# Optimization experiments

Hardware: AMD Instinct MI355X
Metric: run time of the kernel (lower is better)

The kernel has to match this reference:

```python
import jax, jax.numpy as jnp
import numpy as np

V, E, H = 32000, 64, 256
B, T = 8, 512


def _lstm_dir(xs, Wi, Wh, b, reverse):
    """xs: [T, B, D] time-major. Returns hs: [T, B, H].
    Gate layout (custom cell): [f, i, g, o] along the 4H axis."""
    hsz = Wh.shape[0]
    x_proj = jnp.einsum('tbd,dg->tbg', xs, Wi) + b  # precompute input GEMM

    def step(carry, xp_t):
        h, c = carry
        gates = xp_t + h @ Wh
        f = jax.nn.sigmoid(gates[:, :hsz])
        i = jax.nn.sigmoid(gates[:, hsz:2 * hsz])
        g = jnp.tanh(gates[:, 2 * hsz:3 * hsz])
        o = jax.nn.sigmoid(gates[:, 3 * hsz:])
        c = f * c + i * g
        h = o * jnp.tanh(c)
        return (h, c), h

    bsz = xs.shape[1]
    init = (jnp.zeros((bsz, hsz), xs.dtype), jnp.zeros((bsz, hsz), xs.dtype))
    _, hs = jax.lax.scan(step, init, x_proj, reverse=reverse)
    return hs


def setup_inputs() -> dict:
    key = jax.random.key(0)
    ks = jax.random.split(key, 8)
    x = jax.random.randint(ks[0], (B, T), 0, V, dtype=jnp.int32)
    emb = jax.random.normal(ks[1], (V, E), jnp.float32)
    Wi_f = jax.random.normal(ks[2], (E, 4 * H), jnp.float32) / np.sqrt(E)
    Wh_f = jax.random.normal(ks[3], (H, 4 * H), jnp.float32) / np.sqrt(H)
    b_f = jnp.zeros((4 * H,), jnp.float32).at[H:2 * H].set(1.0)
    Wi_b = jax.random.normal(ks[4], (E, 4 * H), jnp.float32) / np.sqrt(E)
    Wh_b = jax.random.normal(ks[5], (H, 4 * H), jnp.float32) / np.sqrt(H)
    b_b = jnp.zeros((4 * H,), jnp.float32).at[H:2 * H].set(1.0)
    W_out = jax.random.normal(ks[6], (2 * H, V), jnp.float32) / np.sqrt(2 * H)
    b_out = jnp.zeros((V,), jnp.float32)
    return {"x": x, "emb": emb, "Wi_f": Wi_f, "Wh_f": Wh_f, "b_f": b_f,
            "Wi_b": Wi_b, "Wh_b": Wh_b, "b_b": b_b,
            "W_out": W_out, "b_out": b_out}


def reference(x, emb, Wi_f, Wh_f, b_f, Wi_b, Wh_b, b_b, W_out, b_out):
    embeds = emb[x]                      # [B, T, E]
    xs = jnp.swapaxes(embeds, 0, 1)      # [T, B, E] time-major for scan
    h_fwd = _lstm_dir(xs, Wi_f, Wh_f, b_f, reverse=False)  # [T, B, H]
    h_bwd = _lstm_dir(xs, Wi_b, Wh_b, b_b, reverse=True)   # [T, B, H]
    h2 = jnp.concatenate([h_fwd, h_bwd], axis=-1)           # [T, B, 2H]
    h2 = jnp.swapaxes(h2, 0, 1)                             # [B, T, 2H]
    logits = jnp.einsum('btd,dv->btv', h2, W_out) + b_out   # [B, T, V]
    return logits
```

## Files before the change

kernel.cpp:

```cpp
#include <hip/hip_runtime.h>
#include <hip/hip_bf16.h>

#define T_LEN 512
#define BATCH 8
#define HID   256
#define G4    1024
#define EMBD  64
#define VOC   32000
#define KDIM  512

typedef __attribute__((ext_vector_type(8))) short bh8;
typedef __attribute__((ext_vector_type(4))) short s4v;
typedef __attribute__((ext_vector_type(4))) float fx4;

__device__ inline unsigned short f2b(float f) {
    unsigned u = __builtin_bit_cast(unsigned, f);
    unsigned r = (u + 0x7fffu + ((u >> 16) & 1u)) >> 16;
    return (unsigned short)r;
}

__device__ inline float sigm(float x) { return 1.f / (1.f + __expf(-x)); }
__device__ inline float tanh_f(float x) {
    float e = __expf(-2.f * fabsf(x));
    float r = (1.f - e) / (1.f + e);
    return copysignf(r, x);
}

__device__ inline void gload_lds16(const void* g, void* l) {
    __builtin_amdgcn_global_load_lds(
        (const __attribute__((address_space(1))) void*)g,
        (__attribute__((address_space(3))) void*)l, 16, 0, 0);
}

__global__ __launch_bounds__(256, 2) void prep_kernel(
    const int* __restrict__ x, const float* __restrict__ emb,
    const float* __restrict__ Wi_f, const float* __restrict__ Wh_f, const float* __restrict__ b_f,
    const float* __restrict__ Wi_b, const float* __restrict__ Wh_b, const float* __restrict__ b_b,
    const float* __restrict__ W_out,
    float* __restrict__ xp_f, float* __restrict__ xp_b,
    unsigned short* __restrict__ WhT_f, unsigned short* __restrict__ WhT_b,
    unsigned short* __restrict__ Wt)
{
    __shared__ float lds[128 * 65];
    __shared__ int xidx[16];
    const int bid = blockIdx.x, tid = threadIdx.x;

    if (bid < 256) {
        const int dir = bid >> 7, b2 = bid & 127;
        const float* Wh = dir ? Wh_b : Wh_f;
        unsigned short* WhT = dir ? WhT_b : WhT_f;
        const int k0 = (b2 >> 4) * 32, n0 = (b2 & 15) * 64;
        for (int it = 0; it < 8; ++it) {
            int idx = it * 256 + tid, kk = idx >> 6, nn = idx & 63;
            lds[kk * 65 + nn] = Wh[(k0 + kk) * G4 + n0 + nn];
        }
        __syncthreads();
        int nn = tid >> 2, kq = (tid & 3) * 8;
        bh8 v;
        #pragma unroll
        for (int j = 0; j < 8; ++j) v[j] = (short)f2b(lds[(kq + j) * 65 + nn]);
        *(bh8*)&WhT[(size_t)(n0 + nn) * HID + k0 + kq] = v;
    } else if (bid < 2256) {
        const int b2 = bid - 256;
        const int k0 = (b2 / 500) * 128, n0 = (b2 % 500) * 64;
        for (int it = 0; it < 32; ++it) {
            int idx = it * 256 + tid, kk = idx >> 6, nn = idx & 63;
            lds[kk * 65 + nn] = W_out[(size_t)(k0 + kk) * VOC + n0 + nn];
        }
        __syncthreads();
        const int kq = (tid & 15) * 8;
        #pragma unroll
        for (int g = 0; g < 4; ++g) {
            int nn = (tid >> 4) + g * 16;
            bh8 v;
            #pragma unroll
            for (int j = 0; j < 8; ++j) v[j] = (short)f2b(lds[(kq + j) * 65 + nn]);
            *(bh8*)&Wt[(size_t)(n0 + nn) * KDIM + k0 + kq] = v;
        }
    } else {
        const int b2 = bid - 2256;
        const int dir = b2 >> 8, rb = b2 & 255;
        const float* Wi = dir ? Wi_b : Wi_f;
        const float* bias = dir ? b_b : b_f;
        float* xp = dir ? xp_b : xp_f;
        const int f0 = rb * 16;
        if (tid < 16) {
            int f = f0 + tid, t = f >> 3, b = f & 7;
            xidx[tid] = x[b * T_LEN + t];
        }
        __syncthreads();
        {
            int rr = tid >> 4, e4 = (tid & 15) * 4;
            const float* er = emb + (size_t)xidx[rr] * EMBD + e4;
            lds[rr * 64 + e4 + 0] = er[0];
            lds[rr * 64 + e4 + 1] = er[1];
            lds[rr * 64 + e4 + 2] = er[2];
            lds[rr * 64 + e4 + 3] = er[3];
        }
        __syncthreads();
        const int g0 = tid * 4;
        float acc[16][4];
        float b0 = bias[g0], b1 = bias[g0 + 1], b2b = bias[g0 + 2], b3 = bias[g0 + 3];
        #pragma unroll
        for (int rr = 0; rr < 16; ++rr) {
            acc[rr][0] = b0; acc[rr][1] = b1; acc[rr][2] = b2b; acc[rr][3] = b3;
        }
        for (int e = 0; e < 64; ++e) {
            const float* wp = Wi + e * G4 + g0;
            float w0 = wp[0], w1 = wp[1], w2 = wp[2], w3 = wp[3];
            #pragma unroll
            for (int rr = 0; rr < 16; ++rr) {
                float xv = lds[rr * 64 + e];
                acc[rr][0] += xv * w0; acc[rr][1] += xv * w1;
                acc[rr][2] += xv * w2; acc[rr][3] += xv * w3;
            }
        }
        #pragma unroll
        for (int rr = 0; rr < 16; ++rr) {
            float* dst = xp + (size_t)(f0 + rr) * G4 + g0;
            dst[0] = acc[rr][0]; dst[1] = acc[rr][1];
            dst[2] = acc[rr][2]; dst[3] = acc[rr][3];
        }
    }
}

__global__ __launch_bounds__(1024, 4) void lstm_kernel(
    const float* __restrict__ xp_f, const float* __restrict__ xp_b,
    const unsigned short* __restrict__ WhT_f, const unsigned short* __restrict__ WhT_b,
    unsigned short* __restrict__ h2)
{
    const int dir = blockIdx.x;
    const float* xp = dir ? xp_b : xp_f;
    const unsigned short* WhT = dir ? WhT_b : WhT_f;
    const int tid = threadIdx.x;
    const int w = tid >> 6, lane = tid & 63, quad = lane >> 4, l15 = lane & 15;
    const int colBase = w * 64;

    __shared__ unsigned short hlds[16 * 264];
    __shared__ float gbuf[4 * 8 * 256];

    for (int i = tid; i < 16 * 264; i += 1024) hlds[i] = 0;

    bh8 bfr[4][8];
    #pragma unroll
    for (int nt = 0; nt < 4; ++nt)
        #pragma unroll
        for (int kt = 0; kt < 8; ++kt)
            bfr[nt][kt] = *(const bh8*)&WhT[(size_t)(colBase + nt * 16 + l15) * HID + kt * 32 + quad * 8];

    fx4 c = (fx4){0.f, 0.f, 0.f, 0.f};
    __syncthreads();

    for (int s = 0; s < T_LEN; ++s) {
        const int t = dir ? (T_LEN - 1 - s) : s;

        fx4 acc[4];
        #pragma unroll
        for (int nt = 0; nt < 4; ++nt) {
            if (quad < 2) {
                const float* p = xp + ((size_t)t * BATCH + quad * 4) * G4 + colBase + nt * 16 + l15;
                acc[nt][0] = p[0]; acc[nt][1] = p[G4]; acc[nt][2] = p[2 * G4]; acc[nt][3] = p[3 * G4];
            } else {
                acc[nt] = (fx4){0.f, 0.f, 0.f, 0.f};
            }
        }
        bh8 af[8];
        #pragma unroll
        for (int kt = 0; kt < 8; ++kt)
            af[kt] = *(const bh8*)&hlds[l15 * 264 + kt * 32 + quad * 8];
        #pragma unroll
        for (int nt = 0; nt < 4; ++nt)
            #pragma unroll
            for (int kt = 0; kt < 8; ++kt)
                acc[nt] = __builtin_amdgcn_mfma_f32_16x16x32_bf16(af[kt], bfr[nt][kt], acc[nt], 0, 0, 0);

        #pragma unroll
        for (int nt = 0; nt < 4; ++nt) {
            const int col = colBase + nt * 16 + l15;
            const int gt = col >> 8, hc = col & 255;
            if (quad < 2) {
                #pragma unroll
                for (int v = 0; v < 4; ++v) {
                    float xv = acc[nt][v];
                    float a = (gt == 2) ? tanh_f(xv) : sigm(xv);
                    gbuf[gt * 2048 + (quad * 4 + v) * 256 + hc] = a;
                }
            }
        }
        __syncthreads();

        if (tid < 512) {
            const int b = tid >> 6, hc0 = (tid & 63) * 4;
            const fx4 fv = *(const fx4*)&gbuf[0 * 2048 + b * 256 + hc0];
            const fx4 iv = *(const fx4*)&gbuf[1 * 2048 + b * 256 + hc0];
            const fx4 gv = *(const fx4*)&gbuf[2 * 2048 + b * 256 + hc0];
            const fx4 ov = *(const fx4*)&gbuf[3 * 2048 + b * 256 + hc0];
            s4v hv;
            #pragma unroll
            for (int j = 0; j < 4; ++j) {
                c[j] = fv[j] * c[j] + iv[j] * gv[j];
                float h = ov[j] * tanh_f(c[j]);
                hv[j] = (short)f2b(h);
            }
            *(s4v*)&hlds[b * 264 + hc0] = hv;
            *(s4v*)&h2[((size_t)b * T_LEN + t) * KDIM + dir * HID + hc0] = hv;
        }
        __syncthreads();
    }
}

__global__ __launch_bounds__(256, 2) void gemm_kernel(
    const unsigned short* __restrict__ A,
    const unsigned short* __restrict__ Bt,
    const float* __restrict__ b_out,
    float* __restrict__ out)
{
    const int bid = blockIdx.x;
    const int nb = bid % 250, mb = bid / 250;
    const int tid = threadIdx.x;
    const int wv = tid >> 6, lane = tid & 63, quad = lane >> 4, l15 = lane & 15;
    const int mrow0 = (wv >> 1) * 64, ncol0 = (wv & 1) * 64;

    __shared__ unsigned short smA[128 * 32];
    __shared__ unsigned short smB[128 * 32];

    fx4 acc[4][4];
    #pragma unroll
    for (int i = 0; i < 4; ++i)
        #pragma unroll
        for (int j = 0; j < 4; ++j) acc[i][j] = (fx4){0.f, 0.f, 0.f, 0.f};

    for (int kb = 0; kb < 16; ++kb) {
        __syncthreads();
        #pragma unroll
        for (int i = 0; i < 2; ++i) {
            const int f = ((i * 4 + wv) * 64 + lane) * 16;
            const int r = f >> 6, cb = f & 63;
            const char* ga = (const char*)A + ((size_t)(mb * 128 + r) * KDIM + kb * 32) * 2 + cb;
            gload_lds16(ga, (char*)smA + (i * 4 + wv) * 1024);
            const char* gb = (const char*)Bt + ((size_t)(nb * 128 + r) * KDIM + kb * 32) * 2 + cb;
            gload_lds16(gb, (char*)smB + (i * 4 + wv) * 1024);
        }
        __syncthreads();
        bh8 a[4], b[4];
        #pragma unroll
        for (int mt = 0; mt < 4; ++mt)
            a[mt] = *(const bh8*)&smA[(mrow0 + mt * 16 + l15) * 32 + quad * 8];
        #pragma unroll
        for (int nt = 0; nt < 4; ++nt)
            b[nt] = *(const bh8*)&smB[(ncol0 + nt * 16 + l15) * 32 + quad * 8];
        #pragma unroll
        for (int mt = 0; mt < 4; ++mt)
            #pragma unroll
            for (int nt = 0; nt < 4; ++nt)
                acc[mt][nt] = __builtin_amdgcn_mfma_f32_16x16x32_bf16(a[mt], b[nt], acc[mt][nt], 0, 0, 0);
    }

    float bia[4];
    #pragma unroll
    for (int nt = 0; nt < 4; ++nt)
        bia[nt] = b_out[nb * 128 + ncol0 + nt * 16 + l15];
    #pragma unroll
    for (int mt = 0; mt < 4; ++mt) {
        const int grow0 = mb * 128 + mrow0 + mt * 16 + quad * 4;
        #pragma unroll
        for (int nt = 0; nt < 4; ++nt) {
            const int gcol = nb * 128 + ncol0 + nt * 16 + l15;
            #pragma unroll
            for (int v = 0; v < 4; ++v)
                out[(size_t)(grow0 + v) * VOC + gcol] = acc[mt][nt][v] + bia[nt];
        }
    }
}

extern "C" void kernel_launch(void* const* d_in, const int* in_sizes, int n_in,
                              void* d_out, int out_size, void* d_ws, size_t ws_size,
                              hipStream_t stream) {
    const int*   x     = (const int*)d_in[0];
    const float* emb   = (const float*)d_in[1];
    const float* Wi_f  = (const float*)d_in[2];
    const float* Wh_f  = (const float*)d_in[3];
    const float* b_f   = (const float*)d_in[4];
    const float* Wi_b  = (const float*)d_in[5];
    const float* Wh_b  = (const float*)d_in[6];
    const float* b_b   = (const float*)d_in[7];
    const float* W_out = (const float*)d_in[8];
    const float* b_out = (const float*)d_in[9];
    float* out = (float*)d_out;

    char* ws = (char*)d_ws;
    float* xp_f          = (float*)(ws);
    float* xp_b          = (float*)(ws + 16777216);
    unsigned short* WhT_f = (unsigned short*)(ws + 33554432);
    unsigned short* WhT_b = (unsigned short*)(ws + 34078720);
    unsigned short* Wt    = (unsigned short*)(ws + 34603008);
    unsigned short* h2    = (unsigned short*)(ws + 67371008);

    prep_kernel<<<2768, 256, 0, stream>>>(x, emb, Wi_f, Wh_f, b_f, Wi_b, Wh_b, b_b,
                                          W_out, xp_f, xp_b, WhT_f, WhT_b, Wt);
    lstm_kernel<<<2, 1024, 0, stream>>>(xp_f, xp_b, WhT_f, WhT_b, h2);
    gemm_kernel<<<8000, 256, 0, stream>>>(h2, Wt, b_out, out);
}
```

Before: 4.764 ms.

## Split each LSTM direction across two workgroups with global h exchange

Each LSTM direction now runs on two 512-thread workgroups, each owning half of the hidden units. All four gates for a hidden unit are kept in one lane so the cell update happens in registers, which removes the gbuf LDS round trip and one barrier per step. The half-h vectors are exchanged every step through global memory, using per-step atomic flags that the workgroups spin on. The xp layout is changed to batch-innermost so the next step's input projection can be prefetched as fx4 loads. The risk is the cross-CU handshake latency on every step, and the spin loop gives up after a fixed iteration count instead of failing.

```diff
diff --git a/kernel.cpp b/kernel.cpp
--- a/kernel.cpp
+++ b/kernel.cpp
@@ -39,13 +39,17 @@
     const float* __restrict__ W_out,
     float* __restrict__ xp_f, float* __restrict__ xp_b,
     unsigned short* __restrict__ WhT_f, unsigned short* __restrict__ WhT_b,
-    unsigned short* __restrict__ Wt)
+    unsigned short* __restrict__ Wt,
+    unsigned int* __restrict__ flags)
 {
     __shared__ float lds[128 * 65];
     __shared__ int xidx[16];
     const int bid = blockIdx.x, tid = threadIdx.x;
 
     if (bid < 256) {
+        if (bid == 0) {
+            for (int i = tid; i < 2 * T_LEN; i += 256) flags[i] = 0;
+        }
         const int dir = bid >> 7, b2 = bid & 127;
         const float* Wh = dir ? Wh_b : Wh_f;
         unsigned short* WhT = dir ? WhT_b : WhT_f;
@@ -117,95 +121,140 @@
         }
         #pragma unroll
         for (int rr = 0; rr < 16; ++rr) {
-            float* dst = xp + (size_t)(f0 + rr) * G4 + g0;
-            dst[0] = acc[rr][0]; dst[1] = acc[rr][1];
-            dst[2] = acc[rr][2]; dst[3] = acc[rr][3];
+            const int f = f0 + rr, tt = f >> 3, bb = f & 7;
+            float* dst = xp + ((size_t)tt * G4 + g0) * 8 + bb;
+            dst[0]  = acc[rr][0];
+            dst[8]  = acc[rr][1];
+            dst[16] = acc[rr][2];
+            dst[24] = acc[rr][3];
         }
     }
 }
 
-__global__ __launch_bounds__(1024, 4) void lstm_kernel(
+__global__ __launch_bounds__(512, 2) void lstm_kernel(
     const float* __restrict__ xp_f, const float* __restrict__ xp_b,
     const unsigned short* __restrict__ WhT_f, const unsigned short* __restrict__ WhT_b,
-    unsigned short* __restrict__ h2)
+    unsigned short* __restrict__ h2,
+    unsigned long long* __restrict__ hxchg,
+    unsigned int* __restrict__ flags)
 {
-    const int dir = blockIdx.x;
+    const int bid = blockIdx.x;
+    const int dir = bid >> 1, half = bid & 1;
     const float* xp = dir ? xp_b : xp_f;
     const unsigned short* WhT = dir ? WhT_b : WhT_f;
     const int tid = threadIdx.x;
     const int w = tid >> 6, lane = tid & 63, quad = lane >> 4, l15 = lane & 15;
-    const int colBase = w * 64;
-
-    __shared__ unsigned short hlds[16 * 264];
-    __shared__ float gbuf[4 * 8 * 256];
-
-    for (int i = tid; i < 16 * 264; i += 1024) hlds[i] = 0;
+    const int hcw = half * 128 + w * 16;
+
+    __shared__ unsigned short hlds[2][8][136];
 
     bh8 bfr[4][8];
     #pragma unroll
     for (int nt = 0; nt < 4; ++nt)
         #pragma unroll
         for (int kt = 0; kt < 8; ++kt)
-            bfr[nt][kt] = *(const bh8*)&WhT[(size_t)(colBase + nt * 16 + l15) * HID + kt * 32 + quad * 8];
+            bfr[nt][kt] = *(const bh8*)&WhT[(size_t)(nt * 256 + hcw + l15) * HID + kt * 32 + quad * 8];
+
+    unsigned int* flg = flags + dir * T_LEN;
+    unsigned long long* hxd = hxchg + (size_t)dir * T_LEN * 512;
 
     fx4 c = (fx4){0.f, 0.f, 0.f, 0.f};
-    __syncthreads();
+
+    const int t0 = dir ? (T_LEN - 1) : 0;
+    fx4 xpre[4];
+    #pragma unroll
+    for (int nt = 0; nt < 4; ++nt)
+        xpre[nt] = (quad < 2)
+            ? *(const fx4*)&xp[((size_t)t0 * G4 + nt * 256 + hcw + l15) * 8 + quad * 4]
+            : (fx4){0.f, 0.f, 0.f, 0.f};
 
     for (int s = 0; s < T_LEN; ++s) {
         const int t = dir ? (T_LEN - 1 - s) : s;
+        const int p = s & 1;
 
         fx4 acc[4];
         #pragma unroll
-        for (int nt = 0; nt < 4; ++nt) {
-            if (quad < 2) {
-                const float* p = xp + ((size_t)t * BATCH + quad * 4) * G4 + colBase + nt * 16 + l15;
-                acc[nt][0] = p[0]; acc[nt][1] = p[G4]; acc[nt][2] = p[2 * G4]; acc[nt][3] = p[3 * G4];
-            } else {
-                acc[nt] = (fx4){0.f, 0.f, 0.f, 0.f};
-            }
-        }
-        bh8 af[8];
-        #pragma unroll
-        for (int kt = 0; kt < 8; ++kt)
-            af[kt] = *(const bh8*)&hlds[l15 * 264 + kt * 32 + quad * 8];
-        #pragma unroll
-        for (int nt = 0; nt < 4; ++nt)
-            #pragma unroll
-            for (int kt = 0; kt < 8; ++kt)
-                acc[nt] = __builtin_amdgcn_mfma_f32_16x16x32_bf16(af[kt], bfr[nt][kt], acc[nt], 0, 0, 0);
-
-        #pragma unroll
-        for (int nt = 0; nt < 4; ++nt) {
-            const int col = colBase + nt * 16 + l15;
-            const int gt = col >> 8, hc = col & 255;
+        for (int nt = 0; nt < 4; ++nt) acc[nt] = xpre[nt];
+
+        if (s + 1 < T_LEN) {
+            const int tn = dir ? (T_LEN - 2 - s) : (s + 1);
             if (quad < 2) {
                 #pragma unroll
-                for (int v = 0; v < 4; ++v) {
-                    float xv = acc[nt][v];
-                    float a = (gt == 2) ? tanh_f(xv) : sigm(xv);
-                    gbuf[gt * 2048 + (quad * 4 + v) * 256 + hc] = a;
-                }
-            }
-        }
-        __syncthreads();
-
-        if (tid < 512) {
-            const int b = tid >> 6, hc0 = (tid & 63) * 4;
-            const fx4 fv = *(const fx4*)&gbuf[0 * 2048 + b * 256 + hc0];
-            const fx4 iv = *(const fx4*)&gbuf[1 * 2048 + b * 256 + hc0];
-            const fx4 gv = *(const fx4*)&gbuf[2 * 2048 + b * 256 + hc0];
-            const fx4 ov = *(const fx4*)&gbuf[3 * 2048 + b * 256 + hc0];
+                for (int nt = 0; nt < 4; ++nt)
+                    xpre[nt] = *(const fx4*)&xp[((size_t)tn * G4 + nt * 256 + hcw + l15) * 8 + quad * 4];
+            }
+        }
+
+        if (s > 0) {
+            const int kb = half * 4;
+            bh8 af[4];
+            #pragma unroll
+            for (int k2 = 0; k2 < 4; ++k2)
+                af[k2] = *(const bh8*)&hlds[p][l15 & 7][k2 * 32 + quad * 8];
+            #pragma unroll
+            for (int k2 = 0; k2 < 4; ++k2)
+                #pragma unroll
+                for (int nt = 0; nt < 4; ++nt)
+                    acc[nt] = __builtin_amdgcn_mfma_f32_16x16x32_bf16(af[k2], bfr[nt][kb + k2], acc[nt], 0, 0, 0);
+
+            unsigned int it = 0;
+            while (__hip_atomic_load(&flg[s - 1], __ATOMIC_RELAXED, __HIP_MEMORY_SCOPE_AGENT) < 2u) {
+                __builtin_amdgcn_s_sleep(1);
+                if (++it > 100000u) break;
+            }
+            asm volatile("" ::: "memory");
+
+            const unsigned long long* hp = hxd + (size_t)(s - 1) * 512 + (1 - half) * 256;
+            const int kbp = (1 - half) * 4;
+            union { unsigned long long q[2]; bh8 v; } pa[4];
+            #pragma unroll
+            for (int k2 = 0; k2 < 4; ++k2) {
+                const int base = (l15 & 7) * 32 + k2 * 8 + quad * 2;
+                pa[k2].q[0] = __hip_atomic_load((unsigned long long*)&hp[base],
+                                                __ATOMIC_RELAXED, __HIP_MEMORY_SCOPE_AGENT);
+                pa[k2].q[1] = __hip_atomic_load((unsigned long long*)&hp[base + 1],
+                                                __ATOMIC_RELAXED, __HIP_MEMORY_SCOPE_AGENT);
+            }
+            #pragma unroll
+            for (int k2 = 0; k2 < 4; ++k2)
+                #pragma unroll
+                for (int nt = 0; nt < 4; ++nt)
+                    acc[nt] = __builtin_amdgcn_mfma_f32_16x16x32_bf16(pa[k2].v, bfr[nt][kbp + k2], acc[nt], 0, 0, 0);
+        }
+
+        if (quad < 2) {
             s4v hv;
             #pragma unroll
-            for (int j = 0; j < 4; ++j) {
-                c[j] = fv[j] * c[j] + iv[j] * gv[j];
-                float h = ov[j] * tanh_f(c[j]);
-                hv[j] = (short)f2b(h);
-            }
-            *(s4v*)&hlds[b * 264 + hc0] = hv;
-            *(s4v*)&h2[((size_t)b * T_LEN + t) * KDIM + dir * HID + hc0] = hv;
-        }
-        __syncthreads();
+            for (int v = 0; v < 4; ++v) {
+                float f = sigm(acc[0][v]);
+                float i = sigm(acc[1][v]);
+                float g = tanh_f(acc[2][v]);
+                float o = sigm(acc[3][v]);
+                c[v] = f * c[v] + i * g;
+                float h = o * tanh_f(c[v]);
+                hv[v] = (short)f2b(h);
+            }
+            #pragma unroll
+            for (int v = 0; v < 4; ++v) {
+                hlds[1 - p][quad * 4 + v][w * 16 + l15] = (unsigned short)hv[v];
+                h2[((size_t)(quad * 4 + v) * T_LEN + t) * KDIM + dir * HID + hcw + l15]
+                    = (unsigned short)hv[v];
+            }
+        }
+
+        __syncthreads();
+
+        if (s + 1 < T_LEN) {
+            if (tid < 256) {
+                unsigned long long vq =
+                    *(const unsigned long long*)&hlds[1 - p][tid >> 5][(tid & 31) * 4];
+                __hip_atomic_store(&hxd[(size_t)s * 512 + half * 256 + tid], vq,
+                                   __ATOMIC_RELAXED, __HIP_MEMORY_SCOPE_AGENT);
+            }
+            __syncthreads();
+            if (tid == 0)
+                __hip_atomic_fetch_add(&flg[s], 1u, __ATOMIC_RELAXED, __HIP_MEMORY_SCOPE_AGENT);
+        }
     }
 }
 
@@ -289,15 +338,17 @@
     float* out = (float*)d_out;
 
     char* ws = (char*)d_ws;
-    float* xp_f          = (float*)(ws);
-    float* xp_b          = (float*)(ws + 16777216);
+    float* xp_f           = (float*)(ws);
+    float* xp_b           = (float*)(ws + 16777216);
     unsigned short* WhT_f = (unsigned short*)(ws + 33554432);
     unsigned short* WhT_b = (unsigned short*)(ws + 34078720);
     unsigned short* Wt    = (unsigned short*)(ws + 34603008);
     unsigned short* h2    = (unsigned short*)(ws + 67371008);
+    unsigned long long* hxchg = (unsigned long long*)(ws + 71565312);
+    unsigned int* flags   = (unsigned int*)(ws + 75759616);
 
     prep_kernel<<<2768, 256, 0, stream>>>(x, emb, Wi_f, Wh_f, b_f, Wi_b, Wh_b, b_b,
-                                          W_out, xp_f, xp_b, WhT_f, WhT_b, Wt);
-    lstm_kernel<<<2, 1024, 0, stream>>>(xp_f, xp_b, WhT_f, WhT_b, h2);
+                                          W_out, xp_f, xp_b, WhT_f, WhT_b, Wt, flags);
+    lstm_kernel<<<4, 512, 0, stream>>>(xp_f, xp_b, WhT_f, WhT_b, h2, hxchg, flags);
     gemm_kernel<<<8000, 256, 0, stream>>>(h2, Wt, b_out, out);
 }
```

New measurement: 6.265 ms. 31.5% more time.

## Remap LSTM gate columns per wave to drop gate buffer and one barrier

Applied to the files above, without the earlier changes.

Each wave now owns 16 hidden units across all four gates, so the cell update runs directly on the MFMA accumulators instead of going through a shared gate buffer. That removes one of the two barriers per timestep. The h state is double-buffered in LDS, the precomputed input projection is relaid out as [t][gate col][batch] for vectorized loads, and the next step's input is prefetched into registers. This costs more register pressure (launch bounds lowered to 1 block per CU, weights pinned in VGPRs via asm) and relies on correct handling of the batch-row mapping for padded MFMA rows.

```diff
diff --git a/kernel.cpp b/kernel.cpp
--- a/kernel.cpp
+++ b/kernel.cpp
@@ -117,14 +117,17 @@
         }
         #pragma unroll
         for (int rr = 0; rr < 16; ++rr) {
-            float* dst = xp + (size_t)(f0 + rr) * G4 + g0;
-            dst[0] = acc[rr][0]; dst[1] = acc[rr][1];
-            dst[2] = acc[rr][2]; dst[3] = acc[rr][3];
+            const int f = f0 + rr, tt = f >> 3, bb = f & 7;
+            float* dst = xp + ((size_t)tt * G4 + g0) * 8 + bb;
+            dst[0]  = acc[rr][0];
+            dst[8]  = acc[rr][1];
+            dst[16] = acc[rr][2];
+            dst[24] = acc[rr][3];
         }
     }
 }
 
-__global__ __launch_bounds__(1024, 4) void lstm_kernel(
+__global__ __launch_bounds__(1024, 1) void lstm_kernel(
     const float* __restrict__ xp_f, const float* __restrict__ xp_b,
     const unsigned short* __restrict__ WhT_f, const unsigned short* __restrict__ WhT_b,
     unsigned short* __restrict__ h2)
@@ -134,77 +137,82 @@
     const unsigned short* WhT = dir ? WhT_b : WhT_f;
     const int tid = threadIdx.x;
     const int w = tid >> 6, lane = tid & 63, quad = lane >> 4, l15 = lane & 15;
-    const int colBase = w * 64;
-
-    __shared__ unsigned short hlds[16 * 264];
-    __shared__ float gbuf[4 * 8 * 256];
-
-    for (int i = tid; i < 16 * 264; i += 1024) hlds[i] = 0;
+    const int hcw = w * 16;
+
+    __shared__ unsigned short hlds[2][8][264];
 
     bh8 bfr[4][8];
     #pragma unroll
-    for (int nt = 0; nt < 4; ++nt)
+    for (int g = 0; g < 4; ++g)
         #pragma unroll
         for (int kt = 0; kt < 8; ++kt)
-            bfr[nt][kt] = *(const bh8*)&WhT[(size_t)(colBase + nt * 16 + l15) * HID + kt * 32 + quad * 8];
+            bfr[g][kt] = *(const bh8*)&WhT[(size_t)(g * 256 + hcw + l15) * HID
+                                            + kt * 32 + quad * 8];
+    #pragma unroll
+    for (int g = 0; g < 4; ++g)
+        #pragma unroll
+        for (int kt = 0; kt < 8; ++kt)
+            asm volatile("" : "+v"(bfr[g][kt]));
 
     fx4 c = (fx4){0.f, 0.f, 0.f, 0.f};
-    __syncthreads();
+
+    const int t0 = dir ? (T_LEN - 1) : 0;
+    fx4 xpre[4];
+    #pragma unroll
+    for (int g = 0; g < 4; ++g)
+        xpre[g] = (quad < 2)
+            ? *(const fx4*)&xp[((size_t)t0 * G4 + g * 256 + hcw + l15) * 8 + quad * 4]
+            : (fx4){0.f, 0.f, 0.f, 0.f};
 
     for (int s = 0; s < T_LEN; ++s) {
         const int t = dir ? (T_LEN - 1 - s) : s;
+        const int p = s & 1;
 
         fx4 acc[4];
         #pragma unroll
-        for (int nt = 0; nt < 4; ++nt) {
-            if (quad < 2) {
-                const float* p = xp + ((size_t)t * BATCH + quad * 4) * G4 + colBase + nt * 16 + l15;
-                acc[nt][0] = p[0]; acc[nt][1] = p[G4]; acc[nt][2] = p[2 * G4]; acc[nt][3] = p[3 * G4];
-            } else {
-                acc[nt] = (fx4){0.f, 0.f, 0.f, 0.f};
-            }
-        }
-        bh8 af[8];
-        #pragma unroll
-        for (int kt = 0; kt < 8; ++kt)
-            af[kt] = *(const bh8*)&hlds[l15 * 264 + kt * 32 + quad * 8];
-        #pragma unroll
-        for (int nt = 0; nt < 4; ++nt)
-            #pragma unroll
-            for (int kt = 0; kt < 8; ++kt)
-                acc[nt] = __builtin_amdgcn_mfma_f32_16x16x32_bf16(af[kt], bfr[nt][kt], acc[nt], 0, 0, 0);
-
-        #pragma unroll
-        for (int nt = 0; nt < 4; ++nt) {
-            const int col = colBase + nt * 16 + l15;
-            const int gt = col >> 8, hc = col & 255;
+        for (int g = 0; g < 4; ++g) acc[g] = xpre[g];
+
+        if (s + 1 < T_LEN) {
+            const int tn = dir ? (T_LEN - 2 - s) : (s + 1);
             if (quad < 2) {
                 #pragma unroll
-                for (int v = 0; v < 4; ++v) {
-                    float xv = acc[nt][v];
-                    float a = (gt == 2) ? tanh_f(xv) : sigm(xv);
-                    gbuf[gt * 2048 + (quad * 4 + v) * 256 + hc] = a;
-                }
+                for (int g = 0; g < 4; ++g)
+                    xpre[g] = *(const fx4*)&xp[((size_t)tn * G4 + g * 256 + hcw + l15) * 8 + quad * 4];
             }
         }
-        __syncthreads();
-
-        if (tid < 512) {
-            const int b = tid >> 6, hc0 = (tid & 63) * 4;
-            const fx4 fv = *(const fx4*)&gbuf[0 * 2048 + b * 256 + hc0];
-            const fx4 iv = *(const fx4*)&gbuf[1 * 2048 + b * 256 + hc0];
-            const fx4 gv = *(const fx4*)&gbuf[2 * 2048 + b * 256 + hc0];
-            const fx4 ov = *(const fx4*)&gbuf[3 * 2048 + b * 256 + hc0];
+
+        if (s > 0) {
+            bh8 af[8];
+            #pragma unroll
+            for (int kt = 0; kt < 8; ++kt)
+                af[kt] = *(const bh8*)&hlds[p][l15 & 7][kt * 32 + quad * 8];
+            #pragma unroll
+            for (int kt = 0; kt < 8; ++kt)
+                #pragma unroll
+                for (int g = 0; g < 4; ++g)
+                    acc[g] = __builtin_amdgcn_mfma_f32_16x16x32_bf16(af[kt], bfr[g][kt], acc[g], 0, 0, 0);
+        }
+
+        if (quad < 2) {
             s4v hv;
             #pragma unroll
-            for (int j = 0; j < 4; ++j) {
-                c[j] = fv[j] * c[j] + iv[j] * gv[j];
-                float h = ov[j] * tanh_f(c[j]);
-                hv[j] = (short)f2b(h);
+            for (int v = 0; v < 4; ++v) {
+                float f = sigm(acc[0][v]);
+                float i = sigm(acc[1][v]);
+                float g = tanh_f(acc[2][v]);
+                float o = sigm(acc[3][v]);
+                c[v] = f * c[v] + i * g;
+                float h = o * tanh_f(c[v]);
+                hv[v] = (short)f2b(h);
             }
-            *(s4v*)&hlds[b * 264 + hc0] = hv;
-            *(s4v*)&h2[((size_t)b * T_LEN + t) * KDIM + dir * HID + hc0] = hv;
-        }
+            #pragma unroll
+            for (int v = 0; v < 4; ++v) {
+                hlds[1 - p][quad * 4 + v][hcw + l15] = (unsigned short)hv[v];
+                h2[((size_t)(quad * 4 + v) * T_LEN + t) * KDIM + dir * HID + hcw + l15]
+                    = (unsigned short)hv[v];
+            }
+        }
+
         __syncthreads();
     }
 }
@@ -289,8 +297,8 @@
     float* out = (float*)d_out;
 
     char* ws = (char*)d_ws;
-    float* xp_f          = (float*)(ws);
-    float* xp_b          = (float*)(ws + 16777216);
+    float* xp_f           = (float*)(ws);
+    float* xp_b           = (float*)(ws + 16777216);
     unsigned short* WhT_f = (unsigned short*)(ws + 33554432);
     unsigned short* WhT_b = (unsigned short*)(ws + 34078720);
     unsigned short* Wt    = (unsigned short*)(ws + 34603008);
```

After: 5.493 ms. 15.3% more time.
